# Optimization experiments

Hardware: AMD Instinct MI355X
Metric: run time of the kernel (lower is better)

Reference implementation:

```python
import jax, jax.numpy as jnp
import numpy as np

B, T, D = 64, 2048, 256


def setup_inputs() -> dict:
    key = jax.random.key(0)
    k_x, k_len, k_w, k_b, k_a = jax.random.split(key, 5)
    xs = jax.random.normal(k_x, (B, T, D), dtype=jnp.float32)
    # ragged lengths -> prefix mask, mimicking per-sample slicing in the torch loop
    lens = jax.random.randint(k_len, (B,), T // 4, T + 1)
    mask = (jnp.arange(T)[None, :] < lens[:, None]).astype(jnp.int32)
    mask2 = jnp.ones((B, T), dtype=jnp.int32)  # unused by the module
    W = jax.random.normal(k_w, (D, D), dtype=jnp.float32) * (1.0 / np.sqrt(D))
    b = jax.random.normal(k_b, (D,), dtype=jnp.float32) * 0.01
    attn = jax.random.normal(k_a, (D,), dtype=jnp.float32)  # nn.Parameter(D,1) squeezed
    return {"xs": xs, "mask": mask, "mask2": mask2, "W": W, "b": b, "attn": attn}


def reference(xs, mask, mask2, W, b, attn):
    # h = tanh(Linear(x)); torch Linear: x @ W.T + b
    h = jnp.tanh(jnp.einsum("btd,ed->bte", xs, W) + b)          # [B,T,D]
    scores = jnp.einsum("btd,d->bt", h, attn)                    # [B,T]
    valid = mask.astype(bool)
    scores = jnp.where(valid, scores, -jnp.inf)                  # softmax over valid frames only
    w = jax.nn.softmax(scores, axis=1)[..., None]                # [B,T,1]
    mu = jnp.sum(xs * w, axis=1)                                 # [B,D]
    var = jnp.maximum(jnp.sum(xs * xs * w, axis=1) - mu * mu, 1e-5)
    return jnp.concatenate([mu, jnp.sqrt(var)], axis=1)          # [B,2D]
```

## Files before the change

### kernel.cpp

```cpp
#include <hip/hip_runtime.h>
#include <hip/hip_bf16.h>
#include <math.h>

#define PB 64
#define PT 2048
#define PD 256
#define PM (PB * PT)

typedef __bf16 bf16x8 __attribute__((ext_vector_type(8)));
typedef short  s16x8  __attribute__((ext_vector_type(8)));
typedef float  f32x4  __attribute__((ext_vector_type(4)));

__device__ __forceinline__ short rne_bf16(float x) {
    unsigned u = __builtin_bit_cast(unsigned, x);
    return (short)((u + 0x7fffu + ((u >> 16) & 1u)) >> 16);
}

__device__ __forceinline__ void split_bf16(float x, short& hi, short& lo) {
    unsigned u = __builtin_bit_cast(unsigned, x);
    hi = (short)(u >> 16);
    float hf = __builtin_bit_cast(float, u & 0xffff0000u);
    lo = rne_bf16(x - hf);
}

__global__ __launch_bounds__(256) void prep_kernel(
    const float* __restrict__ W, short* __restrict__ Whi, short* __restrict__ Wlo)
{
    const int idx = blockIdx.x * 256 + threadIdx.x;
    const int e = idx >> 8;
    const int k = idx & 255;
    short h, l;
    split_bf16(W[idx], h, l);
    const int flat = (((e >> 4) * 8 + (k >> 5)) * 64 + ((k & 31) >> 3) * 16 + (e & 15)) * 8 + (k & 7);
    Whi[flat] = h;
    Wlo[flat] = l;
}

#define SBM 64

__global__ __launch_bounds__(256, 4) void score_kernel(
    const float* __restrict__ xs, const short* __restrict__ Whi,
    const short* __restrict__ Wlo, const float* __restrict__ bias,
    const float* __restrict__ attn, float* __restrict__ scores)
{
    __shared__ short Ah[4 * 8 * 64 * 8];
    __shared__ float sred[4][64];

    const int tid = threadIdx.x;
    const int bm  = blockIdx.x * SBM;

#pragma unroll
    for (int p = 0; p < 8; ++p) {
        const int r  = p * 8 + (tid >> 5);
        const int kb = tid & 31;
        const float4 a0 = *(const float4*)&xs[(bm + r) * PD + kb * 8];
        const float4 a1 = *(const float4*)&xs[(bm + r) * PD + kb * 8 + 4];
        const float f[8] = {a0.x, a0.y, a0.z, a0.w, a1.x, a1.y, a1.z, a1.w};
        s16x8 h;
#pragma unroll
        for (int j = 0; j < 8; ++j) h[j] = rne_bf16(f[j]);
        const int mt = r >> 4, m_loc = r & 15;
        const int kt = kb >> 2, quad = kb & 3;
        const int msw = m_loc ^ (kb & 7);
        *(s16x8*)&Ah[(((mt * 8 + kt) * 64) + quad * 16 + msw) * 8] = h;
    }
    __syncthreads();

    const int lane = tid & 63;
    const int w    = tid >> 6;
    const int quad = lane >> 4;
    const int nl   = lane & 15;

    f32x4 acc[4][4] = {};

#pragma unroll 2
    for (int kt = 0; kt < 8; ++kt) {
        bf16x8 bh[4], bl[4];
#pragma unroll
        for (int n = 0; n < 4; ++n) {
            const int nt = w * 4 + n;
            const int bidx = ((nt * 8 + kt) * 64 + lane) * 8;
            bh[n] = *(const bf16x8*)&Whi[bidx];
            bl[n] = *(const bf16x8*)&Wlo[bidx];
        }
        s16x8 ah[4];
        const int msw = nl ^ ((kt * 4 + quad) & 7);
#pragma unroll
        for (int m = 0; m < 4; ++m)
            ah[m] = *(const s16x8*)&Ah[((m * 8 + kt) * 64 + quad * 16 + msw) * 8];
#pragma unroll
        for (int m = 0; m < 4; ++m) {
            const bf16x8 ahm = __builtin_bit_cast(bf16x8, ah[m]);
#pragma unroll
            for (int n = 0; n < 4; ++n) {
                acc[m][n] = __builtin_amdgcn_mfma_f32_16x16x32_bf16(ahm, bh[n], acc[m][n], 0, 0, 0);
                acc[m][n] = __builtin_amdgcn_mfma_f32_16x16x32_bf16(ahm, bl[n], acc[m][n], 0, 0, 0);
            }
        }
    }

    float bv[4], av[4];
#pragma unroll
    for (int n = 0; n < 4; ++n) {
        const int col = w * 64 + n * 16 + nl;
        bv[n] = bias[col];
        av[n] = attn[col];
    }
#pragma unroll
    for (int m = 0; m < 4; ++m) {
        float rs[4] = {0.f, 0.f, 0.f, 0.f};
#pragma unroll
        for (int n = 0; n < 4; ++n) {
#pragma unroll
            for (int r = 0; r < 4; ++r) {
                const float u  = acc[m][n][r] + bv[n];
                const float e2 = __expf(2.f * u);
                const float th = 1.f - 2.f * __builtin_amdgcn_rcpf(e2 + 1.f);
                rs[r] = fmaf(th, av[n], rs[r]);
            }
        }
#pragma unroll
        for (int off = 1; off < 16; off <<= 1) {
#pragma unroll
            for (int r = 0; r < 4; ++r) rs[r] += __shfl_xor(rs[r], off);
        }
        if (nl == 0) {
#pragma unroll
            for (int r = 0; r < 4; ++r) sred[w][m * 16 + quad * 4 + r] = rs[r];
        }
    }
    __syncthreads();
    if (tid < 64)
        scores[bm + tid] = sred[0][tid] + sred[1][tid] + sred[2][tid] + sred[3][tid];
}

__global__ __launch_bounds__(256) void softmax_kernel(
    const int* __restrict__ mask, float* __restrict__ sw)
{
    const int b    = blockIdx.x;
    const int tid  = threadIdx.x;
    const int lane = tid & 63;
    const int wv   = tid >> 6;
    __shared__ float wred[4];

    float s[8];
    int   v[8];
    float mx = -INFINITY;
#pragma unroll
    for (int i = 0; i < 8; ++i) {
        const int t = i * 256 + tid;
        s[i] = sw[b * PT + t];
        v[i] = mask[b * PT + t];
        if (v[i]) mx = fmaxf(mx, s[i]);
    }
#pragma unroll
    for (int off = 1; off < 64; off <<= 1) mx = fmaxf(mx, __shfl_xor(mx, off));
    if (lane == 0) wred[wv] = mx;
    __syncthreads();
    mx = fmaxf(fmaxf(wred[0], wred[1]), fmaxf(wred[2], wred[3]));
    __syncthreads();

    float p[8];
    float ls = 0.f;
#pragma unroll
    for (int i = 0; i < 8; ++i) {
        p[i] = v[i] ? __expf(s[i] - mx) : 0.f;
        ls += p[i];
    }
#pragma unroll
    for (int off = 1; off < 64; off <<= 1) ls += __shfl_xor(ls, off);
    if (lane == 0) wred[wv] = ls;
    __syncthreads();
    const float inv = 1.f / (wred[0] + wred[1] + wred[2] + wred[3]);
#pragma unroll
    for (int i = 0; i < 8; ++i) sw[b * PT + i * 256 + tid] = p[i] * inv;
}

__global__ __launch_bounds__(256) void moments_kernel(
    const float* __restrict__ xs, const float* __restrict__ w,
    float* __restrict__ part)
{
    const int chunk = blockIdx.x;
    const int b     = blockIdx.y;
    const int tid   = threadIdx.x;
    const int c     = tid & 63;
    const int tq    = tid >> 6;

    __shared__ float  lw[128];
    __shared__ float4 rmu[4][64];
    __shared__ float4 rm2[4][64];

    if (tid < 128) lw[tid] = w[b * PT + chunk * 128 + tid];
    __syncthreads();

    float4 mu = {0.f, 0.f, 0.f, 0.f};
    float4 m2 = {0.f, 0.f, 0.f, 0.f};
    for (int i = 0; i < 32; ++i) {
        const int tl = tq * 32 + i;
        const float wv = lw[tl];
        const float4 x = *(const float4*)&xs[(b * PT + chunk * 128 + tl) * PD + c * 4];
        mu.x = fmaf(wv, x.x, mu.x); mu.y = fmaf(wv, x.y, mu.y);
        mu.z = fmaf(wv, x.z, mu.z); mu.w = fmaf(wv, x.w, mu.w);
        m2.x = fmaf(wv * x.x, x.x, m2.x); m2.y = fmaf(wv * x.y, x.y, m2.y);
        m2.z = fmaf(wv * x.z, x.z, m2.z); m2.w = fmaf(wv * x.w, x.w, m2.w);
    }
    rmu[tq][c] = mu;
    rm2[tq][c] = m2;
    __syncthreads();

    if (tid < 64) {
        float4 smu = rmu[0][tid], sm2 = rm2[0][tid];
        for (int q = 1; q < 4; ++q) {
            const float4 a = rmu[q][tid], d = rm2[q][tid];
            smu.x += a.x; smu.y += a.y; smu.z += a.z; smu.w += a.w;
            sm2.x += d.x; sm2.y += d.y; sm2.z += d.z; sm2.w += d.w;
        }
        const int base = (b * 16 + chunk) * 512;
        *(float4*)&part[base + tid * 4]       = smu;
        *(float4*)&part[base + 256 + tid * 4] = sm2;
    }
}

__global__ __launch_bounds__(256) void finalize_kernel(
    const float* __restrict__ part, float* __restrict__ out)
{
    const int b = blockIdx.x;
    const int d = threadIdx.x;
    float m1 = 0.f, m2 = 0.f;
#pragma unroll
    for (int ch = 0; ch < 16; ++ch) {
        const int base = (b * 16 + ch) * 512;
        m1 += part[base + d];
        m2 += part[base + 256 + d];
    }
    const float var = fmaxf(m2 - m1 * m1, 1e-5f);
    out[b * 512 + d]       = m1;
    out[b * 512 + 256 + d] = sqrtf(var);
}

extern "C" void kernel_launch(void* const* d_in, const int* in_sizes, int n_in,
                              void* d_out, int out_size, void* d_ws, size_t ws_size,
                              hipStream_t stream) {
    const float* xs   = (const float*)d_in[0];
    const int*   mask = (const int*)d_in[1];
    const float* W    = (const float*)d_in[3];
    const float* bias = (const float*)d_in[4];
    const float* attn = (const float*)d_in[5];
    float* out = (float*)d_out;

    float* scores = (float*)d_ws;
    float* part   = scores + PB * PT;
    short* Whi    = (short*)(part + PB * 16 * 512);
    short* Wlo    = Whi + PD * PD;

    prep_kernel<<<PD * PD / 256, 256, 0, stream>>>(W, Whi, Wlo);
    score_kernel<<<PM / SBM, 256, 0, stream>>>(xs, Whi, Wlo, bias, attn, scores);
    softmax_kernel<<<PB, 256, 0, stream>>>(mask, scores);
    moments_kernel<<<dim3(16, PB), 256, 0, stream>>>(xs, scores, part);
    finalize_kernel<<<PB, 256, 0, stream>>>(part, out);
}
```

Before: 253.3 us.

## Fuse score, online-softmax and weighted moments into one tile kernel

Merges the score GEMM, softmax and moment accumulation into a single per-tile kernel. Each tile computes a local max and sum, accumulates unnormalised weighted first and second moments over xs rows while they are likely still in cache, and a finalize kernel rescales the per-tile partials with flash-style max correction. Tiles whose mask is entirely invalid exit early, which skips the GEMM for padded frames. This removes two kernel launches and a second full pass over xs, at the cost of more partial-buffer traffic and extra work inside the score kernel.

```diff
diff --git a/kernel.cpp b/kernel.cpp
--- a/kernel.cpp
+++ b/kernel.cpp
@@ -6,6 +6,9 @@
 #define PT 2048
 #define PD 256
 #define PM (PB * PT)
+#define SBM 64
+#define NT (PM / SBM)
+#define TPB (PT / SBM)
 
 typedef __bf16 bf16x8 __attribute__((ext_vector_type(8)));
 typedef short  s16x8  __attribute__((ext_vector_type(8)));
@@ -36,18 +39,25 @@
     Wlo[flat] = l;
 }
 
-#define SBM 64
-
 __global__ __launch_bounds__(256, 4) void score_kernel(
     const float* __restrict__ xs, const short* __restrict__ Whi,
     const short* __restrict__ Wlo, const float* __restrict__ bias,
-    const float* __restrict__ attn, float* __restrict__ scores)
+    const float* __restrict__ attn, const int* __restrict__ mask,
+    float* __restrict__ stats, float* __restrict__ part)
 {
-    __shared__ short Ah[4 * 8 * 64 * 8];
+    __shared__ __align__(16) short Ah[4 * 8 * 64 * 8];
     __shared__ float sred[4][64];
-
-    const int tid = threadIdx.x;
-    const int bm  = blockIdx.x * SBM;
+    __shared__ float lw[64];
+
+    const int tid  = threadIdx.x;
+    const int tile = blockIdx.x;
+    const int bm   = tile * SBM;
+
+    const int mv = mask[bm + (tid & 63)];
+    if (__ballot(mv != 0) == 0ull) {
+        if (tid == 0) { stats[tile * 2] = -INFINITY; stats[tile * 2 + 1] = 0.f; }
+        return;
+    }
 
 #pragma unroll
     for (int p = 0; p < 8; ++p) {
@@ -130,109 +140,83 @@
         }
     }
     __syncthreads();
-    if (tid < 64)
-        scores[bm + tid] = sred[0][tid] + sred[1][tid] + sred[2][tid] + sred[3][tid];
-}
-
-__global__ __launch_bounds__(256) void softmax_kernel(
-    const int* __restrict__ mask, float* __restrict__ sw)
-{
-    const int b    = blockIdx.x;
-    const int tid  = threadIdx.x;
-    const int lane = tid & 63;
-    const int wv   = tid >> 6;
-    __shared__ float wred[4];
-
-    float s[8];
-    int   v[8];
-    float mx = -INFINITY;
-#pragma unroll
-    for (int i = 0; i < 8; ++i) {
-        const int t = i * 256 + tid;
-        s[i] = sw[b * PT + t];
-        v[i] = mask[b * PT + t];
-        if (v[i]) mx = fmaxf(mx, s[i]);
-    }
-#pragma unroll
-    for (int off = 1; off < 64; off <<= 1) mx = fmaxf(mx, __shfl_xor(mx, off));
-    if (lane == 0) wred[wv] = mx;
-    __syncthreads();
-    mx = fmaxf(fmaxf(wred[0], wred[1]), fmaxf(wred[2], wred[3]));
-    __syncthreads();
-
-    float p[8];
-    float ls = 0.f;
-#pragma unroll
-    for (int i = 0; i < 8; ++i) {
-        p[i] = v[i] ? __expf(s[i] - mx) : 0.f;
-        ls += p[i];
-    }
-#pragma unroll
-    for (int off = 1; off < 64; off <<= 1) ls += __shfl_xor(ls, off);
-    if (lane == 0) wred[wv] = ls;
-    __syncthreads();
-    const float inv = 1.f / (wred[0] + wred[1] + wred[2] + wred[3]);
-#pragma unroll
-    for (int i = 0; i < 8; ++i) sw[b * PT + i * 256 + tid] = p[i] * inv;
-}
-
-__global__ __launch_bounds__(256) void moments_kernel(
-    const float* __restrict__ xs, const float* __restrict__ w,
-    float* __restrict__ part)
-{
-    const int chunk = blockIdx.x;
-    const int b     = blockIdx.y;
-    const int tid   = threadIdx.x;
-    const int c     = tid & 63;
-    const int tq    = tid >> 6;
-
-    __shared__ float  lw[128];
-    __shared__ float4 rmu[4][64];
-    __shared__ float4 rm2[4][64];
-
-    if (tid < 128) lw[tid] = w[b * PT + chunk * 128 + tid];
-    __syncthreads();
-
+
+    if (tid < 64) {
+        float s = sred[0][tid] + sred[1][tid] + sred[2][tid] + sred[3][tid];
+        const bool vld = (mv != 0);
+        s = vld ? s : -INFINITY;
+        float mx = s;
+#pragma unroll
+        for (int off = 1; off < 64; off <<= 1) mx = fmaxf(mx, __shfl_xor(mx, off));
+        const float wt = vld ? __expf(s - mx) : 0.f;
+        float zs = wt;
+#pragma unroll
+        for (int off = 1; off < 64; off <<= 1) zs += __shfl_xor(zs, off);
+        lw[tid] = wt;
+        if (tid == 0) { stats[tile * 2] = mx; stats[tile * 2 + 1] = zs; }
+    }
+    __syncthreads();
+
+    float4* rmu = (float4*)Ah;
+    float4* rm2 = rmu + 4 * 64;
+    const int c  = tid & 63;
+    const int tq = tid >> 6;
     float4 mu = {0.f, 0.f, 0.f, 0.f};
     float4 m2 = {0.f, 0.f, 0.f, 0.f};
-    for (int i = 0; i < 32; ++i) {
-        const int tl = tq * 32 + i;
-        const float wv = lw[tl];
-        const float4 x = *(const float4*)&xs[(b * PT + chunk * 128 + tl) * PD + c * 4];
+#pragma unroll
+    for (int i = 0; i < 16; ++i) {
+        const int r  = tq * 16 + i;
+        const float wv = lw[r];
+        const float4 x = *(const float4*)&xs[(bm + r) * PD + c * 4];
         mu.x = fmaf(wv, x.x, mu.x); mu.y = fmaf(wv, x.y, mu.y);
         mu.z = fmaf(wv, x.z, mu.z); mu.w = fmaf(wv, x.w, mu.w);
         m2.x = fmaf(wv * x.x, x.x, m2.x); m2.y = fmaf(wv * x.y, x.y, m2.y);
         m2.z = fmaf(wv * x.z, x.z, m2.z); m2.w = fmaf(wv * x.w, x.w, m2.w);
     }
-    rmu[tq][c] = mu;
-    rm2[tq][c] = m2;
+    rmu[tq * 64 + c] = mu;
+    rm2[tq * 64 + c] = m2;
     __syncthreads();
 
     if (tid < 64) {
-        float4 smu = rmu[0][tid], sm2 = rm2[0][tid];
+        float4 smu = rmu[tid], sm2 = rm2[tid];
+#pragma unroll
         for (int q = 1; q < 4; ++q) {
-            const float4 a = rmu[q][tid], d = rm2[q][tid];
+            const float4 a = rmu[q * 64 + tid], d = rm2[q * 64 + tid];
             smu.x += a.x; smu.y += a.y; smu.z += a.z; smu.w += a.w;
             sm2.x += d.x; sm2.y += d.y; sm2.z += d.z; sm2.w += d.w;
         }
-        const int base = (b * 16 + chunk) * 512;
+        const int base = tile * 512;
         *(float4*)&part[base + tid * 4]       = smu;
         *(float4*)&part[base + 256 + tid * 4] = sm2;
     }
 }
 
 __global__ __launch_bounds__(256) void finalize_kernel(
-    const float* __restrict__ part, float* __restrict__ out)
+    const float* __restrict__ stats, const float* __restrict__ part,
+    float* __restrict__ out)
 {
     const int b = blockIdx.x;
     const int d = threadIdx.x;
-    float m1 = 0.f, m2 = 0.f;
-#pragma unroll
-    for (int ch = 0; ch < 16; ++ch) {
-        const int base = (b * 16 + ch) * 512;
-        m1 += part[base + d];
-        m2 += part[base + 256 + d];
-    }
+
+    float M = -INFINITY;
+#pragma unroll
+    for (int t = 0; t < TPB; ++t) M = fmaxf(M, stats[(b * TPB + t) * 2]);
+
+    float Z = 0.f, m1 = 0.f, m2 = 0.f;
+#pragma unroll 4
+    for (int t = 0; t < TPB; ++t) {
+        const int g = b * TPB + t;
+        const float zt = stats[g * 2 + 1];
+        if (zt > 0.f) {
+            const float f = __expf(stats[g * 2] - M);
+            Z  = fmaf(zt, f, Z);
+            m1 = fmaf(part[g * 512 + d],       f, m1);
+            m2 = fmaf(part[g * 512 + 256 + d], f, m2);
+        }
+    }
+    const float inv = 1.f / Z;
+    m1 *= inv;
+    m2 *= inv;
     const float var = fmaxf(m2 - m1 * m1, 1e-5f);
     out[b * 512 + d]       = m1;
     out[b * 512 + 256 + d] = sqrtf(var);
@@ -248,14 +232,12 @@
     const float* attn = (const float*)d_in[5];
     float* out = (float*)d_out;
 
-    float* scores = (float*)d_ws;
-    float* part   = scores + PB * PT;
-    short* Whi    = (short*)(part + PB * 16 * 512);
-    short* Wlo    = Whi + PD * PD;
+    float* stats = (float*)d_ws;
+    float* part  = stats + NT * 2;
+    short* Whi   = (short*)(part + NT * 512);
+    short* Wlo   = Whi + PD * PD;
 
     prep_kernel<<<PD * PD / 256, 256, 0, stream>>>(W, Whi, Wlo);
-    score_kernel<<<PM / SBM, 256, 0, stream>>>(xs, Whi, Wlo, bias, attn, scores);
-    softmax_kernel<<<PB, 256, 0, stream>>>(mask, scores);
-    moments_kernel<<<dim3(16, PB), 256, 0, stream>>>(xs, scores, part);
-    finalize_kernel<<<PB, 256, 0, stream>>>(part, out);
-}
+    score_kernel<<<NT, 256, 0, stream>>>(xs, Whi, Wlo, bias, attn, mask, stats, part);
+    finalize_kernel<<<PB, 256, 0, stream>>>(stats, part, out);
+}
```

After: 229.2 us. 9.5% less time.
